# Kernel optimization log

Hardware: AMD Instinct MI355X
Metric: run time of the kernel (lower is better)

## Reference

```python
import jax, jax.numpy as jnp
import numpy as np

B, D, N, S = 1024, 512, 500000, 32768


def setup_inputs() -> dict:
    key = jax.random.key(0)
    k1, k2, k3 = jax.random.split(key, 3)
    inputs = jax.random.normal(k1, (B, D), dtype=jnp.float32)
    # Linear(D, N) init: uniform(-0.05, 0.05) weight, zero bias
    weight = jax.random.uniform(k2, (N, D), dtype=jnp.float32, minval=-0.05, maxval=0.05)
    bias = jnp.zeros((N,), dtype=jnp.float32)
    sample_ids = jax.random.randint(k3, (S,), 0, N, dtype=jnp.int64)
    return {"inputs": inputs, "weight": weight, "bias": bias, "sample_ids": sample_ids}


def reference(inputs, weight, bias, sample_ids):
    # Gather retrieved class embeddings: [S, D] and their biases [S]
    sample_weights = weight[sample_ids]
    sample_bias = bias[sample_ids]
    # Sampled logits: inputs @ sample_weights.T + bias  -> [B, S]
    # (matches sample_weights.matmul(inputs.t()).t() + sample_bias in torch)
    logits = jnp.einsum("bd,sd->bs", inputs, sample_weights) + sample_bias
    return logits
```

## Files before the change

kernel.cpp:

```cpp
#include <hip/hip_runtime.h>
#include <stdint.h>

#define B_DIM 1024
#define D_DIM 512
#define S_DIM 32768

typedef __attribute__((ext_vector_type(8))) short bf16x8;
typedef __attribute__((ext_vector_type(4))) float f32x4;
typedef __attribute__((ext_vector_type(8))) unsigned short u16x8;

#define AS1 __attribute__((address_space(1)))
#define AS3 __attribute__((address_space(3)))

__device__ __forceinline__ unsigned short f2bf(float f) {
  union { float f; uint32_t u; } x; x.f = f;
  uint32_t r = x.u + 0x7fffu + ((x.u >> 16) & 1u);
  return (unsigned short)(r >> 16);
}

#define GATHER_BLOCKS (S_DIM / 4)
#define CONV_BLOCKS (B_DIM * D_DIM / 8 / 256)

__global__ __launch_bounds__(256) void prep(const float* __restrict__ W,
                                            const float* __restrict__ bias,
                                            const int* __restrict__ ids,
                                            const float* __restrict__ A,
                                            unsigned short* __restrict__ Wg,
                                            unsigned short* __restrict__ Ab,
                                            float* __restrict__ bg) {
  if (blockIdx.x < GATHER_BLOCKS) {
    int gid = blockIdx.x * 256 + threadIdx.x;
    int s = gid >> 6;
    int c = (gid & 63) * 8;
    int sid = ids[s];
    const float* src = W + (size_t)sid * D_DIM + c;
    float4 v0 = *(const float4*)src;
    float4 v1 = *(const float4*)(src + 4);
    u16x8 o;
    o[0] = f2bf(v0.x); o[1] = f2bf(v0.y); o[2] = f2bf(v0.z); o[3] = f2bf(v0.w);
    o[4] = f2bf(v1.x); o[5] = f2bf(v1.y); o[6] = f2bf(v1.z); o[7] = f2bf(v1.w);
    *(u16x8*)(Wg + (size_t)s * D_DIM + c) = o;
    if ((gid & 63) == 0) bg[s] = bias[sid];
  } else {
    int gid = (blockIdx.x - GATHER_BLOCKS) * 256 + threadIdx.x;
    const float* src = A + (size_t)gid * 8;
    float4 v0 = *(const float4*)src;
    float4 v1 = *(const float4*)(src + 4);
    u16x8 o;
    o[0] = f2bf(v0.x); o[1] = f2bf(v0.y); o[2] = f2bf(v0.z); o[3] = f2bf(v0.w);
    o[4] = f2bf(v1.x); o[5] = f2bf(v1.y); o[6] = f2bf(v1.z); o[7] = f2bf(v1.w);
    *(u16x8*)(Ab + (size_t)gid * 8) = o;
  }
}

#define BM 128
#define BN 128
#define BK 64
#define NKT (D_DIM / BK)
#define A_BYTES (BM * BK * 2)
#define B_BYTES (BN * BK * 2)
#define BUFBYTES (A_BYTES + B_BYTES)

__global__ __launch_bounds__(512, 4) void gemm_bias(const unsigned short* __restrict__ Ab,
                                                    const unsigned short* __restrict__ Wg,
                                                    const float* __restrict__ bg,
                                                    float* __restrict__ out) {
  __shared__ __attribute__((aligned(16))) char lds[2 * BUFBYTES];

  const int tid = threadIdx.x;
  const int lane = tid & 63;
  const int w = tid >> 6;
  const int wr = w >> 2;
  const int wc = w & 3;
  const int lq = lane >> 4;
  const int l16 = lane & 15;

  int id = ((blockIdx.x & 7) << 8) | (blockIdx.x >> 3);
  const int bm = id & 7;
  const int bn = id >> 3;
  const int m0 = bm * BM;
  const int n0 = bn * BN;

  f32x4 acc[4][2];
#pragma unroll
  for (int m = 0; m < 4; ++m)
#pragma unroll
    for (int n = 0; n < 2; ++n)
      acc[m][n] = (f32x4)0.0f;

  auto stage = [&](int kt) {
    char* ldsA = lds + (kt & 1) * BUFBYTES;
    char* ldsB = ldsA + A_BYTES;
#pragma unroll
    for (int j = 0; j < 2; ++j) {
      const int Pb = j * 8192 + w * 1024;
      const int P = Pb + lane * 16;
      const int L = P ^ (((P >> 7) & 7) << 4);
      const char* srcA = (const char*)Ab +
          (size_t)(m0 + (L >> 7)) * (D_DIM * 2) + kt * (BK * 2) + (L & 127);
      __builtin_amdgcn_global_load_lds((const AS1 void*)srcA,
                                       (AS3 void*)(ldsA + Pb), 16, 0, 0);
      const char* srcB = (const char*)Wg +
          (size_t)(n0 + (L >> 7)) * (D_DIM * 2) + kt * (BK * 2) + (L & 127);
      __builtin_amdgcn_global_load_lds((const AS1 void*)srcB,
                                       (AS3 void*)(ldsB + Pb), 16, 0, 0);
    }
  };

  stage(0);

  const int swz = (l16 & 7) << 4;

#pragma unroll
  for (int kt = 0; kt < NKT; ++kt) {
    __builtin_amdgcn_sched_barrier(0);
    if (kt < NKT - 1) {
      stage(kt + 1);
      __builtin_amdgcn_sched_barrier(0);
      asm volatile("s_waitcnt vmcnt(4)" ::: "memory");
    } else {
      asm volatile("s_waitcnt vmcnt(0)" ::: "memory");
    }
    __builtin_amdgcn_s_barrier();
    __builtin_amdgcn_sched_barrier(0);

    const char* ldsA = lds + (kt & 1) * BUFBYTES;
    const char* ldsB = ldsA + A_BYTES;

#pragma unroll
    for (int kk = 0; kk < 2; ++kk) {
      bf16x8 af[4], bv[2];
#pragma unroll
      for (int m = 0; m < 4; ++m) {
        const int row = wr * 64 + m * 16 + l16;
        const int byte = row * 128 + (kk * 32 + lq * 8) * 2;
        af[m] = *(const bf16x8*)(ldsA + (byte ^ swz));
      }
#pragma unroll
      for (int n = 0; n < 2; ++n) {
        const int row = wc * 32 + n * 16 + l16;
        const int byte = row * 128 + (kk * 32 + lq * 8) * 2;
        bv[n] = *(const bf16x8*)(ldsB + (byte ^ swz));
      }
      __builtin_amdgcn_s_setprio(1);
#pragma unroll
      for (int m = 0; m < 4; ++m)
#pragma unroll
        for (int n = 0; n < 2; ++n)
          acc[m][n] = __builtin_amdgcn_mfma_f32_16x16x32_bf16(af[m], bv[n],
                                                              acc[m][n], 0, 0, 0);
      __builtin_amdgcn_s_setprio(0);
    }

    __builtin_amdgcn_sched_barrier(0);
    __builtin_amdgcn_s_barrier();
  }

  const int lrow = lq * 4;
#pragma unroll
  for (int n = 0; n < 2; ++n) {
    const int col = n0 + wc * 32 + n * 16 + l16;
    const float bvv = bg[col];
#pragma unroll
    for (int m = 0; m < 4; ++m) {
      const int rbase = m0 + wr * 64 + m * 16 + lrow;
#pragma unroll
      for (int r = 0; r < 4; ++r) {
        out[(size_t)(rbase + r) * S_DIM + col] = acc[m][n][r] + bvv;
      }
    }
  }
}

extern "C" void kernel_launch(void* const* d_in, const int* in_sizes, int n_in,
                              void* d_out, int out_size, void* d_ws, size_t ws_size,
                              hipStream_t stream) {
  const float* inp  = (const float*)d_in[0];
  const float* W    = (const float*)d_in[1];
  const float* bias = (const float*)d_in[2];
  const int*   ids  = (const int*)d_in[3];
  float* out = (float*)d_out;

  unsigned short* Wg = (unsigned short*)d_ws;
  unsigned short* Ab = (unsigned short*)((char*)d_ws +
                        (size_t)S_DIM * D_DIM * 2);
  float* bg = (float*)((char*)d_ws +
                        (size_t)S_DIM * D_DIM * 2 + (size_t)B_DIM * D_DIM * 2);

  prep<<<GATHER_BLOCKS + CONV_BLOCKS, 256, 0, stream>>>(W, bias, ids, inp, Wg, Ab, bg);

  dim3 grid((B_DIM / BM) * (S_DIM / BN));
  gemm_bias<<<grid, 512, 0, stream>>>(Ab, Wg, bg, out);
}
```

Before: 64.09 us.

## Enlarge GEMM tiles to 256x256 with half-tile staged LDS pipeline

Doubles the block tile to 256x256 with a 128x64 per-wave subtile, which cuts global and LDS traffic per MFMA. Staging now works on half-K units, interleaved with compute phases and gated by a table-driven vmcnt wait schedule, and uses a new rotation-based LDS swizzle. The cost is a 128 KB LDS footprint, 128 accumulator registers, lower occupancy (launch bounds 2) and only 512 blocks, so there are fewer waves to hide latency and a risk of tail imbalance.

```diff
diff --git a/kernel.cpp b/kernel.cpp
--- a/kernel.cpp
+++ b/kernel.cpp
@@ -53,15 +53,27 @@
   }
 }
 
-#define BM 128
-#define BN 128
+#define BM 256
+#define BN 256
 #define BK 64
 #define NKT (D_DIM / BK)
-#define A_BYTES (BM * BK * 2)
-#define B_BYTES (BN * BK * 2)
-#define BUFBYTES (A_BYTES + B_BYTES)
-
-__global__ __launch_bounds__(512, 4) void gemm_bias(const unsigned short* __restrict__ Ab,
+#define AREG 32768
+#define BUFBYTES 65536
+
+#define VMC(n) asm volatile("s_waitcnt vmcnt(" #n ")" ::: "memory")
+__device__ __forceinline__ void vmcnt_sw(int n) {
+  switch (n) {
+    case 0:  VMC(0); break;
+    case 2:  VMC(2); break;
+    case 4:  VMC(4); break;
+    case 6:  VMC(6); break;
+    case 8:  VMC(8); break;
+    case 10: VMC(10); break;
+    default: VMC(12); break;
+  }
+}
+
+__global__ __launch_bounds__(512, 2) void gemm_bias(const unsigned short* __restrict__ Ab,
                                                     const unsigned short* __restrict__ Wg,
                                                     const float* __restrict__ bg,
                                                     float* __restrict__ out) {
@@ -70,100 +82,122 @@
   const int tid = threadIdx.x;
   const int lane = tid & 63;
   const int w = tid >> 6;
-  const int wr = w >> 2;
-  const int wc = w & 3;
+  const int wm = w >> 2;
+  const int wn = w & 3;
   const int lq = lane >> 4;
   const int l16 = lane & 15;
 
-  int id = ((blockIdx.x & 7) << 8) | (blockIdx.x >> 3);
-  const int bm = id & 7;
-  const int bn = id >> 3;
-  const int m0 = bm * BM;
-  const int n0 = bn * BN;
-
-  f32x4 acc[4][2];
-#pragma unroll
-  for (int m = 0; m < 4; ++m)
-#pragma unroll
-    for (int n = 0; n < 2; ++n)
+  const int id = ((blockIdx.x & 7) << 6) | (blockIdx.x >> 3);
+  const int m0 = (id & 3) * BM;
+  const int n0 = (id >> 2) * BN;
+
+  f32x4 acc[8][4];
+#pragma unroll
+  for (int m = 0; m < 8; ++m)
+#pragma unroll
+    for (int n = 0; n < 4; ++n)
       acc[m][n] = (f32x4)0.0f;
 
-  auto stage = [&](int kt) {
-    char* ldsA = lds + (kt & 1) * BUFBYTES;
-    char* ldsB = ldsA + A_BYTES;
+  auto stage_unit = [&](int tile, int isB, int half) {
+    if (tile >= NKT) return;
+    char* ubase = lds + (tile & 1) * BUFBYTES + isB * AREG + half * 16384;
+    const unsigned short* gsrc = isB ? Wg : Ab;
+    const int org = isB ? n0 : m0;
 #pragma unroll
     for (int j = 0; j < 2; ++j) {
-      const int Pb = j * 8192 + w * 1024;
-      const int P = Pb + lane * 16;
-      const int L = P ^ (((P >> 7) & 7) << 4);
-      const char* srcA = (const char*)Ab +
-          (size_t)(m0 + (L >> 7)) * (D_DIM * 2) + kt * (BK * 2) + (L & 127);
-      __builtin_amdgcn_global_load_lds((const AS1 void*)srcA,
-                                       (AS3 void*)(ldsA + Pb), 16, 0, 0);
-      const char* srcB = (const char*)Wg +
-          (size_t)(n0 + (L >> 7)) * (D_DIM * 2) + kt * (BK * 2) + (L & 127);
-      __builtin_amdgcn_global_load_lds((const AS1 void*)srcB,
-                                       (AS3 void*)(ldsB + Pb), 16, 0, 0);
+      const int slot = j * 512 + w * 64 + lane;
+      const int row = slot >> 2;
+      const int q = ((slot & 3) - (row >> 1)) & 3;
+      const unsigned short* src = gsrc + (size_t)(org + row) * D_DIM
+                                  + tile * BK + half * 32 + q * 8;
+      __builtin_amdgcn_global_load_lds((const AS1 void*)src,
+                                       (AS3 void*)(ubase + j * 8192 + w * 1024),
+                                       16, 0, 0);
     }
   };
 
-  stage(0);
-
-  const int swz = (l16 & 7) << 4;
-
-#pragma unroll
-  for (int kt = 0; kt < NKT; ++kt) {
-    __builtin_amdgcn_sched_barrier(0);
-    if (kt < NKT - 1) {
-      stage(kt + 1);
-      __builtin_amdgcn_sched_barrier(0);
-      asm volatile("s_waitcnt vmcnt(4)" ::: "memory");
-    } else {
-      asm volatile("s_waitcnt vmcnt(0)" ::: "memory");
+  stage_unit(0, 0, 0);
+  stage_unit(0, 1, 0);
+  stage_unit(0, 0, 1);
+  stage_unit(0, 1, 1);
+  stage_unit(1, 0, 0);
+  stage_unit(1, 1, 0);
+  VMC(8);
+  __builtin_amdgcn_s_barrier();
+
+  static const int NTAB[4][8] = {
+    {12, 8, 12, 8, 12, 8, 12, 8},
+    {12, 8, 12, 8, 12, 8, 12, 8},
+    {12, 8, 12, 8, 12, 8, 12, 8},
+    {12, 8,  8, 4,  6, 0,  2, 0},
+  };
+
+#pragma unroll
+  for (int i = 0; i < NKT / 2; ++i) {
+#pragma unroll
+    for (int t01 = 0; t01 < 2; ++t01) {
+      const int tile = 2 * i + t01;
+      const char* bufb = lds + (tile & 1) * BUFBYTES;
+#pragma unroll
+      for (int h = 0; h < 2; ++h) {
+        bf16x8 bf[4];
+#pragma unroll
+        for (int mg = 0; mg < 2; ++mg) {
+          const int ph = t01 * 4 + h * 2 + mg;
+
+          bf16x8 af[4];
+          const char* Abase = bufb + h * 16384;
+#pragma unroll
+          for (int j = 0; j < 4; ++j) {
+            const int rl = wm * 128 + mg * 64 + j * 16 + l16;
+            const int blk = (rl << 2) + ((lq + (rl >> 1)) & 3);
+            af[j] = *(const bf16x8*)(Abase + (blk << 4));
+          }
+          if (mg == 0) {
+            const char* Bbase = bufb + AREG + h * 16384;
+#pragma unroll
+            for (int j = 0; j < 4; ++j) {
+              const int cl = wn * 64 + j * 16 + l16;
+              const int blk = (cl << 2) + ((lq + (cl >> 1)) & 3);
+              bf[j] = *(const bf16x8*)(Bbase + (blk << 4));
+            }
+          }
+
+          {
+            const int stile = 2 * i + 1 + (ph >= 2) + (ph >= 6);
+            const int sisB = ph & 1;
+            const int shalf = 1 - ((ph >> 1) & 1);
+            stage_unit(stile, sisB, shalf);
+          }
+          __builtin_amdgcn_sched_barrier(0);
+          vmcnt_sw(NTAB[i][ph]);
+          __builtin_amdgcn_s_barrier();
+          asm volatile("s_waitcnt lgkmcnt(0)" ::: "memory");
+          __builtin_amdgcn_sched_barrier(0);
+
+          __builtin_amdgcn_s_setprio(1);
+#pragma unroll
+          for (int j = 0; j < 4; ++j)
+#pragma unroll
+            for (int n = 0; n < 4; ++n)
+              acc[mg * 4 + j][n] = __builtin_amdgcn_mfma_f32_16x16x32_bf16(
+                  af[j], bf[n], acc[mg * 4 + j][n], 0, 0, 0);
+          __builtin_amdgcn_s_setprio(0);
+          __builtin_amdgcn_sched_barrier(0);
+          __builtin_amdgcn_s_barrier();
+        }
+      }
     }
-    __builtin_amdgcn_s_barrier();
-    __builtin_amdgcn_sched_barrier(0);
-
-    const char* ldsA = lds + (kt & 1) * BUFBYTES;
-    const char* ldsB = ldsA + A_BYTES;
-
-#pragma unroll
-    for (int kk = 0; kk < 2; ++kk) {
-      bf16x8 af[4], bv[2];
-#pragma unroll
-      for (int m = 0; m < 4; ++m) {
-        const int row = wr * 64 + m * 16 + l16;
-        const int byte = row * 128 + (kk * 32 + lq * 8) * 2;
-        af[m] = *(const bf16x8*)(ldsA + (byte ^ swz));
-      }
-#pragma unroll
-      for (int n = 0; n < 2; ++n) {
-        const int row = wc * 32 + n * 16 + l16;
-        const int byte = row * 128 + (kk * 32 + lq * 8) * 2;
-        bv[n] = *(const bf16x8*)(ldsB + (byte ^ swz));
-      }
-      __builtin_amdgcn_s_setprio(1);
-#pragma unroll
-      for (int m = 0; m < 4; ++m)
-#pragma unroll
-        for (int n = 0; n < 2; ++n)
-          acc[m][n] = __builtin_amdgcn_mfma_f32_16x16x32_bf16(af[m], bv[n],
-                                                              acc[m][n], 0, 0, 0);
-      __builtin_amdgcn_s_setprio(0);
-    }
-
-    __builtin_amdgcn_sched_barrier(0);
-    __builtin_amdgcn_s_barrier();
   }
 
   const int lrow = lq * 4;
 #pragma unroll
-  for (int n = 0; n < 2; ++n) {
-    const int col = n0 + wc * 32 + n * 16 + l16;
+  for (int n = 0; n < 4; ++n) {
+    const int col = n0 + wn * 64 + n * 16 + l16;
     const float bvv = bg[col];
 #pragma unroll
-    for (int m = 0; m < 4; ++m) {
-      const int rbase = m0 + wr * 64 + m * 16 + lrow;
+    for (int m = 0; m < 8; ++m) {
+      const int rbase = m0 + wm * 128 + m * 16 + lrow;
 #pragma unroll
       for (int r = 0; r < 4; ++r) {
         out[(size_t)(rbase + r) * S_DIM + col] = acc[m][n][r] + bvv;
```

New measurement: 72.05 us. 1.12x slower.

## Fuse weight row gather and bf16 conversion into the GEMM B-tile staging

Applied to the files above, without the earlier changes.

Removes the separate prep pass that gathered sampled weight rows into a bf16 workspace. Each GEMM block now loads its fp32 weight rows by id directly into registers, converts them with packed bf16 conversion instructions and writes them into swizzled LDS, with a register prefetch one k-tile ahead. Bias is read through ids in the epilogue. This avoids writing and re-reading the 32 MB bf16 gathered matrix. In exchange, each of the 8 M-blocks re-reads the fp32 weight rows, and the pipeline now waits on vmcnt(0) each iteration, which reduces overlap.

```diff
diff --git a/kernel.cpp b/kernel.cpp
--- a/kernel.cpp
+++ b/kernel.cpp
@@ -18,39 +18,22 @@
   return (unsigned short)(r >> 16);
 }
 
-#define GATHER_BLOCKS (S_DIM / 4)
-#define CONV_BLOCKS (B_DIM * D_DIM / 8 / 256)
-
-__global__ __launch_bounds__(256) void prep(const float* __restrict__ W,
-                                            const float* __restrict__ bias,
-                                            const int* __restrict__ ids,
-                                            const float* __restrict__ A,
-                                            unsigned short* __restrict__ Wg,
-                                            unsigned short* __restrict__ Ab,
-                                            float* __restrict__ bg) {
-  if (blockIdx.x < GATHER_BLOCKS) {
-    int gid = blockIdx.x * 256 + threadIdx.x;
-    int s = gid >> 6;
-    int c = (gid & 63) * 8;
-    int sid = ids[s];
-    const float* src = W + (size_t)sid * D_DIM + c;
-    float4 v0 = *(const float4*)src;
-    float4 v1 = *(const float4*)(src + 4);
-    u16x8 o;
-    o[0] = f2bf(v0.x); o[1] = f2bf(v0.y); o[2] = f2bf(v0.z); o[3] = f2bf(v0.w);
-    o[4] = f2bf(v1.x); o[5] = f2bf(v1.y); o[6] = f2bf(v1.z); o[7] = f2bf(v1.w);
-    *(u16x8*)(Wg + (size_t)s * D_DIM + c) = o;
-    if ((gid & 63) == 0) bg[s] = bias[sid];
-  } else {
-    int gid = (blockIdx.x - GATHER_BLOCKS) * 256 + threadIdx.x;
-    const float* src = A + (size_t)gid * 8;
-    float4 v0 = *(const float4*)src;
-    float4 v1 = *(const float4*)(src + 4);
-    u16x8 o;
-    o[0] = f2bf(v0.x); o[1] = f2bf(v0.y); o[2] = f2bf(v0.z); o[3] = f2bf(v0.w);
-    o[4] = f2bf(v1.x); o[5] = f2bf(v1.y); o[6] = f2bf(v1.z); o[7] = f2bf(v1.w);
-    *(u16x8*)(Ab + (size_t)gid * 8) = o;
-  }
+__device__ __forceinline__ uint32_t cvtpk(float a, float b) {
+  uint32_t r;
+  asm("v_cvt_pk_bf16_f32 %0, %1, %2" : "=v"(r) : "v"(a), "v"(b));
+  return r;
+}
+
+__global__ __launch_bounds__(256) void conv_a(const float* __restrict__ A,
+                                              unsigned short* __restrict__ Ab) {
+  int gid = blockIdx.x * 256 + threadIdx.x;
+  const float* src = A + (size_t)gid * 8;
+  float4 v0 = *(const float4*)src;
+  float4 v1 = *(const float4*)(src + 4);
+  u16x8 o;
+  o[0] = f2bf(v0.x); o[1] = f2bf(v0.y); o[2] = f2bf(v0.z); o[3] = f2bf(v0.w);
+  o[4] = f2bf(v1.x); o[5] = f2bf(v1.y); o[6] = f2bf(v1.z); o[7] = f2bf(v1.w);
+  *(u16x8*)(Ab + (size_t)gid * 8) = o;
 }
 
 #define BM 128
@@ -61,10 +44,11 @@
 #define B_BYTES (BN * BK * 2)
 #define BUFBYTES (A_BYTES + B_BYTES)
 
-__global__ __launch_bounds__(512, 4) void gemm_bias(const unsigned short* __restrict__ Ab,
-                                                    const unsigned short* __restrict__ Wg,
-                                                    const float* __restrict__ bg,
-                                                    float* __restrict__ out) {
+__global__ __launch_bounds__(512, 4) void gemm_fused(const unsigned short* __restrict__ Ab,
+                                                     const float* __restrict__ W,
+                                                     const float* __restrict__ bias,
+                                                     const int* __restrict__ ids,
+                                                     float* __restrict__ out) {
   __shared__ __attribute__((aligned(16))) char lds[2 * BUFBYTES];
 
   const int tid = threadIdx.x;
@@ -81,6 +65,13 @@
   const int m0 = bm * BM;
   const int n0 = bn * BN;
 
+  const int srow = tid >> 2;
+  const int sseg = tid & 3;
+  const int myid = ids[n0 + srow];
+  const float* wbase = W + (size_t)myid * D_DIM + sseg * 16;
+  const int sbyte = srow * 128 + sseg * 32;
+  const int sswz = (srow & 7) << 4;
+
   f32x4 acc[4][2];
 #pragma unroll
   for (int m = 0; m < 4; ++m)
@@ -88,9 +79,8 @@
     for (int n = 0; n < 2; ++n)
       acc[m][n] = (f32x4)0.0f;
 
-  auto stage = [&](int kt) {
+  auto stageA = [&](int kt) {
     char* ldsA = lds + (kt & 1) * BUFBYTES;
-    char* ldsB = ldsA + A_BYTES;
 #pragma unroll
     for (int j = 0; j < 2; ++j) {
       const int Pb = j * 8192 + w * 1024;
@@ -100,14 +90,35 @@
           (size_t)(m0 + (L >> 7)) * (D_DIM * 2) + kt * (BK * 2) + (L & 127);
       __builtin_amdgcn_global_load_lds((const AS1 void*)srcA,
                                        (AS3 void*)(ldsA + Pb), 16, 0, 0);
-      const char* srcB = (const char*)Wg +
-          (size_t)(n0 + (L >> 7)) * (D_DIM * 2) + kt * (BK * 2) + (L & 127);
-      __builtin_amdgcn_global_load_lds((const AS1 void*)srcB,
-                                       (AS3 void*)(ldsB + Pb), 16, 0, 0);
     }
   };
 
-  stage(0);
+  float4 q0, q1, q2, q3;
+  auto loadB = [&](int kt) {
+    const float* p = wbase + kt * BK;
+    q0 = *(const float4*)(p + 0);
+    q1 = *(const float4*)(p + 4);
+    q2 = *(const float4*)(p + 8);
+    q3 = *(const float4*)(p + 12);
+  };
+  auto writeB = [&](int kt) {
+    char* bb = lds + (kt & 1) * BUFBYTES + A_BYTES;
+    int4 w0, w1;
+    w0.x = cvtpk(q0.x, q0.y); w0.y = cvtpk(q0.z, q0.w);
+    w0.z = cvtpk(q1.x, q1.y); w0.w = cvtpk(q1.z, q1.w);
+    w1.x = cvtpk(q2.x, q2.y); w1.y = cvtpk(q2.z, q2.w);
+    w1.z = cvtpk(q3.x, q3.y); w1.w = cvtpk(q3.z, q3.w);
+    *(int4*)(bb + (sbyte ^ sswz)) = w0;
+    *(int4*)(bb + ((sbyte + 16) ^ sswz)) = w1;
+  };
+
+  loadB(0);
+  stageA(0);
+  asm volatile("s_waitcnt vmcnt(2)" ::: "memory");
+  writeB(0);
+  asm volatile("s_waitcnt vmcnt(0)" ::: "memory");
+  asm volatile("s_waitcnt lgkmcnt(0)" ::: "memory");
+  __builtin_amdgcn_s_barrier();
 
   const int swz = (l16 & 7) << 4;
 
@@ -115,13 +126,9 @@
   for (int kt = 0; kt < NKT; ++kt) {
     __builtin_amdgcn_sched_barrier(0);
     if (kt < NKT - 1) {
-      stage(kt + 1);
-      __builtin_amdgcn_sched_barrier(0);
-      asm volatile("s_waitcnt vmcnt(4)" ::: "memory");
-    } else {
-      asm volatile("s_waitcnt vmcnt(0)" ::: "memory");
-    }
-    __builtin_amdgcn_s_barrier();
+      loadB(kt + 1);
+      stageA(kt + 1);
+    }
     __builtin_amdgcn_sched_barrier(0);
 
     const char* ldsA = lds + (kt & 1) * BUFBYTES;
@@ -151,16 +158,23 @@
                                                               acc[m][n], 0, 0, 0);
       __builtin_amdgcn_s_setprio(0);
     }
-
     __builtin_amdgcn_sched_barrier(0);
-    __builtin_amdgcn_s_barrier();
+
+    if (kt < NKT - 1) {
+      asm volatile("s_waitcnt vmcnt(2)" ::: "memory");
+      writeB(kt + 1);
+      __builtin_amdgcn_sched_barrier(0);
+      asm volatile("s_waitcnt vmcnt(0)" ::: "memory");
+      asm volatile("s_waitcnt lgkmcnt(0)" ::: "memory");
+      __builtin_amdgcn_s_barrier();
+    }
   }
 
   const int lrow = lq * 4;
 #pragma unroll
   for (int n = 0; n < 2; ++n) {
     const int col = n0 + wc * 32 + n * 16 + l16;
-    const float bvv = bg[col];
+    const float bvv = bias[ids[col]];
 #pragma unroll
     for (int m = 0; m < 4; ++m) {
       const int rbase = m0 + wr * 64 + m * 16 + lrow;
@@ -181,14 +195,10 @@
   const int*   ids  = (const int*)d_in[3];
   float* out = (float*)d_out;
 
-  unsigned short* Wg = (unsigned short*)d_ws;
-  unsigned short* Ab = (unsigned short*)((char*)d_ws +
-                        (size_t)S_DIM * D_DIM * 2);
-  float* bg = (float*)((char*)d_ws +
-                        (size_t)S_DIM * D_DIM * 2 + (size_t)B_DIM * D_DIM * 2);
-
-  prep<<<GATHER_BLOCKS + CONV_BLOCKS, 256, 0, stream>>>(W, bias, ids, inp, Wg, Ab, bg);
+  unsigned short* Ab = (unsigned short*)d_ws;
+
+  conv_a<<<(B_DIM * D_DIM / 8) / 256, 256, 0, stream>>>(inp, Ab);
 
   dim3 grid((B_DIM / BM) * (S_DIM / BN));
-  gemm_bias<<<grid, 512, 0, stream>>>(Ab, Wg, bg, out);
-}
+  gemm_fused<<<grid, 512, 0, stream>>>(Ab, W, bias, ids, out);
+}
```

Result: slower. 89.20 us (+39.2%).

## Switch GEMM to BK=32 triple-buffered LDS pipeline with prefetch distance two

Applied to the files above, without the earlier changes.

Halves the K tile to 32 and uses three LDS buffers so global-to-LDS loads run two iterations ahead instead of one. The LDS layout is reorganized to pack two rows per 128-byte line with an XOR swizzle, and per-lane offsets are precomputed. Launch bounds now request 6 blocks per CU. The aim is deeper memory latency hiding and higher occupancy, at the cost of twice as many barrier-synchronized iterations, each with less MFMA work.

```diff
diff --git a/kernel.cpp b/kernel.cpp
--- a/kernel.cpp
+++ b/kernel.cpp
@@ -55,17 +55,16 @@
 
 #define BM 128
 #define BN 128
-#define BK 64
+#define BK 32
 #define NKT (D_DIM / BK)
-#define A_BYTES (BM * BK * 2)
-#define B_BYTES (BN * BK * 2)
-#define BUFBYTES (A_BYTES + B_BYTES)
+#define REGB 8192
+#define BUFBYTES (2 * REGB)
 
-__global__ __launch_bounds__(512, 4) void gemm_bias(const unsigned short* __restrict__ Ab,
+__global__ __launch_bounds__(512, 6) void gemm_bias(const unsigned short* __restrict__ Ab,
                                                     const unsigned short* __restrict__ Wg,
                                                     const float* __restrict__ bg,
                                                     float* __restrict__ out) {
-  __shared__ __attribute__((aligned(16))) char lds[2 * BUFBYTES];
+  __shared__ __attribute__((aligned(16))) char lds[3 * BUFBYTES];
 
   const int tid = threadIdx.x;
   const int lane = tid & 63;
@@ -76,10 +75,8 @@
   const int l16 = lane & 15;
 
   int id = ((blockIdx.x & 7) << 8) | (blockIdx.x >> 3);
-  const int bm = id & 7;
-  const int bn = id >> 3;
-  const int m0 = bm * BM;
-  const int n0 = bn * BN;
+  const int m0 = (id & 7) * BM;
+  const int n0 = (id >> 3) * BN;
 
   f32x4 acc[4][2];
 #pragma unroll
@@ -88,69 +85,65 @@
     for (int n = 0; n < 2; ++n)
       acc[m][n] = (f32x4)0.0f;
 
+  const int sp = tid >> 3;
+  const int ssl = (tid & 7) ^ (sp & 7);
+  const int srow = (sp << 1) + (ssl >> 2);
+  const int scb = (ssl & 3) << 4;
+  const char* sA0 = (const char*)Ab + (size_t)(m0 + srow) * (D_DIM * 2) + scb;
+  const char* sB0 = (const char*)Wg + (size_t)(n0 + srow) * (D_DIM * 2) + scb;
+
   auto stage = [&](int kt) {
-    char* ldsA = lds + (kt & 1) * BUFBYTES;
-    char* ldsB = ldsA + A_BYTES;
-#pragma unroll
-    for (int j = 0; j < 2; ++j) {
-      const int Pb = j * 8192 + w * 1024;
-      const int P = Pb + lane * 16;
-      const int L = P ^ (((P >> 7) & 7) << 4);
-      const char* srcA = (const char*)Ab +
-          (size_t)(m0 + (L >> 7)) * (D_DIM * 2) + kt * (BK * 2) + (L & 127);
-      __builtin_amdgcn_global_load_lds((const AS1 void*)srcA,
-                                       (AS3 void*)(ldsA + Pb), 16, 0, 0);
-      const char* srcB = (const char*)Wg +
-          (size_t)(n0 + (L >> 7)) * (D_DIM * 2) + kt * (BK * 2) + (L & 127);
-      __builtin_amdgcn_global_load_lds((const AS1 void*)srcB,
-                                       (AS3 void*)(ldsB + Pb), 16, 0, 0);
-    }
+    char* base = lds + (kt % 3) * BUFBYTES + w * 1024;
+    __builtin_amdgcn_global_load_lds((const AS1 void*)(sA0 + kt * (BK * 2)),
+                                     (AS3 void*)base, 16, 0, 0);
+    __builtin_amdgcn_global_load_lds((const AS1 void*)(sB0 + kt * (BK * 2)),
+                                     (AS3 void*)(base + REGB), 16, 0, 0);
   };
 
+  int aoff[4], boff[2];
+#pragma unroll
+  for (int m = 0; m < 4; ++m) {
+    const int r = wr * 64 + m * 16 + l16;
+    aoff[m] = (r >> 1) * 128 + ((((r & 1) << 6) + (lq << 4)) ^ (((r >> 1) & 7) << 4));
+  }
+#pragma unroll
+  for (int n = 0; n < 2; ++n) {
+    const int r = wc * 32 + n * 16 + l16;
+    boff[n] = REGB + (r >> 1) * 128 + ((((r & 1) << 6) + (lq << 4)) ^ (((r >> 1) & 7) << 4));
+  }
+
   stage(0);
+  stage(1);
 
-  const int swz = (l16 & 7) << 4;
-
-#pragma unroll
   for (int kt = 0; kt < NKT; ++kt) {
     __builtin_amdgcn_sched_barrier(0);
-    if (kt < NKT - 1) {
-      stage(kt + 1);
+    if (kt < NKT - 2) {
+      stage(kt + 2);
       __builtin_amdgcn_sched_barrier(0);
       asm volatile("s_waitcnt vmcnt(4)" ::: "memory");
+    } else if (kt == NKT - 2) {
+      asm volatile("s_waitcnt vmcnt(2)" ::: "memory");
     } else {
       asm volatile("s_waitcnt vmcnt(0)" ::: "memory");
     }
     __builtin_amdgcn_s_barrier();
     __builtin_amdgcn_sched_barrier(0);
 
-    const char* ldsA = lds + (kt & 1) * BUFBYTES;
-    const char* ldsB = ldsA + A_BYTES;
+    const char* bufb = lds + (kt % 3) * BUFBYTES;
+    bf16x8 af[4], bv[2];
+#pragma unroll
+    for (int m = 0; m < 4; ++m) af[m] = *(const bf16x8*)(bufb + aoff[m]);
+#pragma unroll
+    for (int n = 0; n < 2; ++n) bv[n] = *(const bf16x8*)(bufb + boff[n]);
 
+    __builtin_amdgcn_s_setprio(1);
 #pragma unroll
-    for (int kk = 0; kk < 2; ++kk) {
-      bf16x8 af[4], bv[2];
+    for (int m = 0; m < 4; ++m)
 #pragma unroll
-      for (int m = 0; m < 4; ++m) {
-        const int row = wr * 64 + m * 16 + l16;
-        const int byte = row * 128 + (kk * 32 + lq * 8) * 2;
-        af[m] = *(const bf16x8*)(ldsA + (byte ^ swz));
-      }
-#pragma unroll
-      for (int n = 0; n < 2; ++n) {
-        const int row = wc * 32 + n * 16 + l16;
-        const int byte = row * 128 + (kk * 32 + lq * 8) * 2;
-        bv[n] = *(const bf16x8*)(ldsB + (byte ^ swz));
-      }
-      __builtin_amdgcn_s_setprio(1);
-#pragma unroll
-      for (int m = 0; m < 4; ++m)
-#pragma unroll
-        for (int n = 0; n < 2; ++n)
-          acc[m][n] = __builtin_amdgcn_mfma_f32_16x16x32_bf16(af[m], bv[n],
-                                                              acc[m][n], 0, 0, 0);
-      __builtin_amdgcn_s_setprio(0);
-    }
+      for (int n = 0; n < 2; ++n)
+        acc[m][n] = __builtin_amdgcn_mfma_f32_16x16x32_bf16(af[m], bv[n],
+                                                            acc[m][n], 0, 0, 0);
+    __builtin_amdgcn_s_setprio(0);
 
     __builtin_amdgcn_sched_barrier(0);
     __builtin_amdgcn_s_barrier();
```

Result: slower. 73.00 us (+13.9%).
